# Optimization experiments

Hardware: AMD Instinct MI355X
Metric: run time of the kernel (lower is better)

The kernel has to match this reference:

```python
import jax, jax.numpy as jnp
import numpy as np

B = 1024      # batch
HG = 28       # grid side (28x28 image -> graph)
N = HG * HG   # 784 nodes per sample
K = 70        # node_sampled (relaxed categorical classes)
GCN_OUT = 48
H_DIM = 400
Z = 70
IMG = 784
TEMP = 0.5


def _grid_edges():
    idx = np.arange(N).reshape(HG, HG)
    src = np.concatenate([idx[:, :-1].ravel(), idx[:, 1:].ravel(), idx[:-1, :].ravel(), idx[1:, :].ravel()])
    dst = np.concatenate([idx[:, 1:].ravel(), idx[:, :-1].ravel(), idx[1:, :].ravel(), idx[:-1, :].ravel()])
    loop = np.arange(N)
    return (np.concatenate([src, loop]).astype(np.int32),
            np.concatenate([dst, loop]).astype(np.int32))


def _lin(key, fi, fo):
    kw, kb = jax.random.split(key)
    s = 1.0 / np.sqrt(fi)
    return (jax.random.uniform(kw, (fi, fo), jnp.float32, -s, s),
            jax.random.uniform(kb, (fo,), jnp.float32, -s, s))


def setup_inputs() -> dict:
    key = jax.random.key(0)
    ks = jax.random.split(key, 16)
    src, dst = _grid_edges()
    u = jax.random.uniform(ks[2], (B, N, K), jnp.float32, 1e-6, 1.0 - 1e-6)
    inp = {
        'nodes': jax.random.normal(ks[0], (B, N, 2), jnp.float32),
        'logits': jax.random.normal(ks[1], (B, N, K), jnp.float32),
        'gumbel': -jnp.log(-jnp.log(u)),
        'eps': jax.random.normal(ks[3], (B, Z), jnp.float32),
    }
    inp['W1'], inp['b1'] = _lin(ks[4], 2, 16)
    inp['W2'], inp['b2'] = _lin(ks[5], 16, 32)
    inp['W3'], inp['b3'] = _lin(ks[6], 32, GCN_OUT)
    inp['We1'], inp['be1'] = _lin(ks[7], K * GCN_OUT, H_DIM)
    inp['We2'], inp['be2'] = _lin(ks[8], H_DIM, H_DIM)
    inp['Wmu'], inp['bmu'] = _lin(ks[9], H_DIM, Z)
    inp['Wvar'], inp['bvar'] = _lin(ks[10], H_DIM, Z)
    inp['Wd1'], inp['bd1'] = _lin(ks[11], Z, H_DIM)
    inp['Wd2'], inp['bd2'] = _lin(ks[12], H_DIM, IMG)
    inp['edge_src'] = jnp.asarray(src)
    inp['edge_dst'] = jnp.asarray(dst)
    return inp


def reference(nodes, logits, gumbel, eps,
              W1, b1, W2, b2, W3, b3,
              We1, be1, We2, be2,
              Wmu, bmu, Wvar, bvar,
              Wd1, bd1, Wd2, bd2,
              edge_src, edge_dst):
    # symmetric GCN normalization with self loops (already in edge list)
    deg = jnp.zeros((N,), nodes.dtype).at[edge_dst].add(1.0)
    dinv = jax.lax.rsqrt(deg)
    norm = dinv[edge_src] * dinv[edge_dst]  # [E]

    def gcn(h, W, b):
        h = h @ W                                   # [B,N,Fout]
        msg = h[:, edge_src] * norm[None, :, None]  # gather + scale, [B,E,Fout]
        return jnp.zeros_like(h).at[:, edge_dst].add(msg) + b

    h = jax.nn.relu(gcn(nodes, W1, b1))
    h = jax.nn.relu(gcn(h, W2, b2))
    h = jax.nn.relu(gcn(h, W3, b3))            # [B,N,48]

    # RelaxedOneHotCategorical(temp=0.5).rsample() == gumbel-softmax
    sample = jax.nn.softmax((logits + gumbel) / TEMP, axis=-1)  # [B,N,K]
    g = jnp.einsum('bnk,bnf->bkf', sample, h).reshape(h.shape[0], K * GCN_OUT)

    # encoder MLP + reparameterize
    e = jax.nn.relu(g @ We1 + be1)
    e = jax.nn.relu(e @ We2 + be2)
    mu = e @ Wmu + bmu
    var = jax.nn.softplus(e @ Wvar + bvar)
    z = mu + eps * jnp.sqrt(var + 1e-10)

    # decoder
    d = jax.nn.relu(z @ Wd1 + bd1)
    x_rec = jax.nn.sigmoid(d @ Wd2 + bd2)      # [B,784]
    return x_rec
```

## Files before the change

### kernel.cpp

```cpp
#include <hip/hip_runtime.h>
#include <hip/hip_bf16.h>


#define BB 1024
#define HG 28
#define NN 784
#define KK 70
#define F3 48
#define HD 400
#define ZD 70
#define IMGD 784

typedef __hip_bfloat16 bf16;
typedef __attribute__((ext_vector_type(8))) short s8v;
typedef __attribute__((ext_vector_type(4))) float f32x4;

__device__ __forceinline__ float dinv_ij(int i, int j){
  int deg = 1 + (i>0) + (i<HG-1) + (j>0) + (j<HG-1);
  return rsqrtf((float)deg);
}

__device__ __forceinline__ unsigned pk2(float a, float b){
  union { bf16 h; unsigned short u; } ua, ub;
  ua.h = __float2bfloat16(a); ub.h = __float2bfloat16(b);
  return ((unsigned)ub.u << 16) | ua.u;
}

__device__ __forceinline__ short bfbits(float v){
  union { bf16 h; short s; } u; u.h = __float2bfloat16(v); return u.s;
}

#define SYNC_LDS() do {                                   \
    asm volatile("" ::: "memory");                        \
    asm volatile("s_waitcnt lgkmcnt(0)" ::: "memory");    \
    __builtin_amdgcn_s_barrier();                         \
    asm volatile("" ::: "memory");                        \
  } while(0)

__global__ __launch_bounds__(256, 2)
void gcn_fused(const float* __restrict__ nodes,
               const float* __restrict__ W1, const float* __restrict__ b1,
               const float* __restrict__ W2, const float* __restrict__ b2,
               const float* __restrict__ W3, const float* __restrict__ b3,
               bf16* __restrict__ h3){
  __shared__ __align__(16) char smem[73216];
  float* regA = (float*)smem;
  float* regB = (float*)(smem + 36288);
  float* wbuf = (float*)(smem + 64512);
  float* W1s = wbuf;          float* b1s = wbuf + 32;
  float* W2s = wbuf + 48;     float* b2s = wbuf + 560;
  float* W3s = wbuf + 592;    float* b3s = wbuf + 2128;

  int tid = threadIdx.x;
  if (tid < 32)  W1s[tid] = W1[tid];
  if (tid < 16)  b1s[tid] = b1[tid];
  for (int t = tid; t < 512;  t += 256) W2s[t] = W2[t];
  if (tid < 32)  b2s[tid] = b2[tid];
  for (int t = tid; t < 1536; t += 256) W3s[t] = W3[t];
  if (tid < 48)  b3s[tid] = b3[tid];

  int b = blockIdx.x >> 2, s = blockIdx.x & 3;
  int base3 = s*7;
  int base2 = base3 - 1;
  int base1 = base3 - 2;
  const float* nb = nodes + (size_t)b*NN*2;
  __syncthreads();

  {
    float* h1s = regA;
    for (int t = tid; t < 308; t += 256){
      int lr = t/28, j = t - lr*28;
      int r = base1 + lr;
      float o[16] __attribute__((aligned(16)));
      if (r < 0 || r >= HG){
        #pragma unroll
        for (int f=0; f<16; f++) o[f] = 0.f;
      } else {
        float dn = dinv_ij(r,j);
        float a0 = dn*nb[(r*HG+j)*2+0], a1 = dn*nb[(r*HG+j)*2+1];
        if (r > 0)   { float w=dinv_ij(r-1,j); a0 += w*nb[((r-1)*HG+j)*2]; a1 += w*nb[((r-1)*HG+j)*2+1]; }
        if (r < HG-1){ float w=dinv_ij(r+1,j); a0 += w*nb[((r+1)*HG+j)*2]; a1 += w*nb[((r+1)*HG+j)*2+1]; }
        if (j > 0)   { float w=dinv_ij(r,j-1); a0 += w*nb[(r*HG+j-1)*2];   a1 += w*nb[(r*HG+j-1)*2+1]; }
        if (j < HG-1){ float w=dinv_ij(r,j+1); a0 += w*nb[(r*HG+j+1)*2];   a1 += w*nb[(r*HG+j+1)*2+1]; }
        a0 *= dn; a1 *= dn;
        #pragma unroll
        for (int f=0; f<16; f++) o[f] = fmaxf(a0*W1s[f] + a1*W1s[16+f] + b1s[f], 0.f);
      }
      float* dst = h1s + t*20;
      #pragma unroll
      for (int qq=0; qq<4; qq++) *(float4*)(dst + 4*qq) = *(float4*)&o[4*qq];
    }
  }
  __syncthreads();

  if (tid < 252){
    const float* h1s = regA;
    float* agg1 = regB;
    int lr = tid/28, j = tid - lr*28;
    int r = base2 + lr;
    float o[16] __attribute__((aligned(16)));
    if (r < 0 || r >= HG){
      #pragma unroll
      for (int f=0; f<16; f++) o[f] = 0.f;
    } else {
      int ln = (lr+1)*28 + j;
      float dn = dinv_ij(r,j);
      float wu = dinv_ij(r-1,j), wd = dinv_ij(r+1,j);
      float wl = (j>0)    ? dinv_ij(r,j-1) : 0.f;
      float wr = (j<HG-1) ? dinv_ij(r,j+1) : 0.f;
      const float* pc = h1s + ln*20;
      #pragma unroll
      for (int qq=0; qq<4; qq++){
        float4 vc = *(const float4*)(pc + 4*qq);
        float4 vu = *(const float4*)(pc - 28*20 + 4*qq);
        float4 vd = *(const float4*)(pc + 28*20 + 4*qq);
        float4 vl = *(const float4*)(pc - 20 + 4*qq);
        float4 vr = *(const float4*)(pc + 20 + 4*qq);
        o[4*qq+0] = dn*(dn*vc.x + wu*vu.x + wd*vd.x + wl*vl.x + wr*vr.x);
        o[4*qq+1] = dn*(dn*vc.y + wu*vu.y + wd*vd.y + wl*vl.y + wr*vr.y);
        o[4*qq+2] = dn*(dn*vc.z + wu*vu.z + wd*vd.z + wl*vl.z + wr*vr.z);
        o[4*qq+3] = dn*(dn*vc.w + wu*vu.w + wd*vd.w + wl*vl.w + wr*vr.w);
      }
    }
    float* dst = agg1 + tid*20;
    #pragma unroll
    for (int qq=0; qq<4; qq++) *(float4*)(dst + 4*qq) = *(float4*)&o[4*qq];
  }
  __syncthreads();

  {
    const float* agg1 = regB;
    float* h2s = regA;
    int tx = tid & 7, ty = tid >> 3;
    float4 w2r[16];
    #pragma unroll
    for (int fi=0; fi<16; fi++) w2r[fi] = *(const float4*)&W2s[fi*32 + tx*4];
    float4 bb = *(const float4*)&b2s[tx*4];
    #pragma unroll
    for (int i=0; i<8; i++){
      int n = ty + 32*i;
      if (n < 252){
        float af[16] __attribute__((aligned(16)));
        const float* ap = agg1 + n*20;
        #pragma unroll
        for (int qq=0; qq<4; qq++) *(float4*)&af[4*qq] = *(const float4*)(ap + 4*qq);
        float4 acc = bb;
        #pragma unroll
        for (int fi=0; fi<16; fi++){
          float a = af[fi];
          acc.x += a*w2r[fi].x; acc.y += a*w2r[fi].y;
          acc.z += a*w2r[fi].z; acc.w += a*w2r[fi].w;
        }
        acc.x = fmaxf(acc.x,0.f); acc.y = fmaxf(acc.y,0.f);
        acc.z = fmaxf(acc.z,0.f); acc.w = fmaxf(acc.w,0.f);
        *(float4*)&h2s[n*36 + tx*4] = acc;
      }
    }
  }
  __syncthreads();

  if (tid < 196){
    const float* h2s = regA;
    float* agg2 = regB;
    int lr = tid/28, j = tid - lr*28;
    int r = base3 + lr;
    int ln = (lr+1)*28 + j;
    float dn = dinv_ij(r,j);
    float wu = dinv_ij(r-1,j), wd = dinv_ij(r+1,j);
    float wl = (j>0)    ? dinv_ij(r,j-1) : 0.f;
    float wr = (j<HG-1) ? dinv_ij(r,j+1) : 0.f;
    const float* pc = h2s + ln*36;
    float* dst = agg2 + tid*36;
    #pragma unroll
    for (int qq=0; qq<8; qq++){
      float4 vc = *(const float4*)(pc + 4*qq);
      float4 vu = *(const float4*)(pc - 28*36 + 4*qq);
      float4 vd = *(const float4*)(pc + 28*36 + 4*qq);
      float4 vl = *(const float4*)(pc - 36 + 4*qq);
      float4 vr = *(const float4*)(pc + 36 + 4*qq);
      float4 o;
      o.x = dn*(dn*vc.x + wu*vu.x + wd*vd.x + wl*vl.x + wr*vr.x);
      o.y = dn*(dn*vc.y + wu*vu.y + wd*vd.y + wl*vl.y + wr*vr.y);
      o.z = dn*(dn*vc.z + wu*vu.z + wd*vd.z + wl*vl.z + wr*vr.z);
      o.w = dn*(dn*vc.w + wu*vu.w + wd*vd.w + wl*vl.w + wr*vr.w);
      *(float4*)(dst + 4*qq) = o;
    }
  }
  __syncthreads();

  {
    bf16* h3buf = (bf16*)regA;
    if (tid < 252){
      const float* agg2 = regB;
      int tx = tid % 12, ty = tid / 12;
      float4 w3r[32];
      #pragma unroll
      for (int fi=0; fi<32; fi++) w3r[fi] = *(const float4*)&W3s[fi*48 + tx*4];
      float4 bb = *(const float4*)&b3s[tx*4];
      #pragma unroll
      for (int i=0; i<10; i++){
        int n = ty + 21*i;
        if (n < 196){
          float af[32] __attribute__((aligned(16)));
          const float* ap = agg2 + n*36;
          #pragma unroll
          for (int qq=0; qq<8; qq++) *(float4*)&af[4*qq] = *(const float4*)(ap + 4*qq);
          float4 acc = bb;
          #pragma unroll
          for (int fi=0; fi<32; fi++){
            float a = af[fi];
            acc.x += a*w3r[fi].x; acc.y += a*w3r[fi].y;
            acc.z += a*w3r[fi].z; acc.w += a*w3r[fi].w;
          }
          uint2 pv;
          pv.x = pk2(fmaxf(acc.x,0.f), fmaxf(acc.y,0.f));
          pv.y = pk2(fmaxf(acc.z,0.f), fmaxf(acc.w,0.f));
          *(uint2*)((char*)h3buf + n*112 + tx*8) = pv;
        }
      }
    }
  }
  __syncthreads();

  {
    const char* h3buf = (const char*)regA;
    uint4* dst = (uint4*)(h3 + ((size_t)b*NN + base3*28)*F3);
    for (int t = tid; t < 1176; t += 256){
      int n = t/6, gq = t - n*6;
      dst[t] = *(const uint4*)(h3buf + n*112 + gq*16);
    }
  }
}

__global__ __launch_bounds__(256, 4)
void einsum_mfma_kernel(const float* __restrict__ logits, const float* __restrict__ gumbel,
                        const bf16* __restrict__ h3, float* __restrict__ g){
  __shared__ __align__(16) unsigned smemS[7488];
  const int SLO = 2880, HTO = 5760;

  int b = blockIdx.x, tid = threadIdx.x;
  int l = tid & 63, w = tid >> 6;
  int n_loc = tid >> 2, q = tid & 3;
  int kstart = q << 4;
  int kcnt = (q < 3) ? 16 : 22;
  int kc2 = kcnt >> 1;
  int m_pair = tid >> 3;
  int half = (tid >> 2) & 1;
  int ks = w >> 1, mh = w & 1;
  int mtoff = mh ? 3 : 0, mtcnt = mh ? 2 : 3;

  for (int t = tid; t < 720; t += 256){
    int bb2 = t >= 360, r = t - bb2*360;
    if (bb2) smemS[SLO + 2520 + r] = 0u;
    else     smemS[2520 + r] = 0u;
  }

  f32x4 acc[3][3];
  #pragma unroll
  for (int mt=0; mt<3; mt++)
    #pragma unroll
    for (int bt=0; bt<3; bt++) acc[mt][bt] = (f32x4){0.f,0.f,0.f,0.f};

  float2 lx[11], gx[11];
  uint2 hA0, hB0, hA1, hB1;
  int hm0 = tid/12, hj0 = tid - hm0*12;
  int tt1 = tid + 256;
  int hm1 = tt1/12, hj1 = tt1 - hm1*12;

  auto issue_into = [&](int c){
    int c0 = c << 6;
    int node = c0 + n_loc;
    bool v = node < NN;
    const float* lp = logits + ((size_t)b*NN + node)*KK + kstart;
    const float* gp = gumbel + ((size_t)b*NN + node)*KK + kstart;
    int nld = (q < 3) ? 8 : 11;
    #pragma unroll
    for (int s=0; s<11; s++){
      bool a = v && (s < nld);
      lx[s] = a ? *(const float2*)(lp + 2*s) : (float2){0.f,0.f};
      gx[s] = a ? *(const float2*)(gp + 2*s) : (float2){0.f,0.f};
    }
    bool vA0 = (c0 + 2*hm0)     < NN;
    bool vB0 = (c0 + 2*hm0 + 1) < NN;
    const uint2* p0 = (const uint2*)(h3 + ((size_t)b*NN + c0 + 2*hm0)*F3 + 4*hj0);
    hA0 = vA0 ? p0[0]  : (uint2){0u,0u};
    hB0 = vB0 ? p0[12] : (uint2){0u,0u};
    if (tid < 128){
      bool vA1 = (c0 + 2*hm1)     < NN;
      bool vB1 = (c0 + 2*hm1 + 1) < NN;
      const uint2* p1 = (const uint2*)(h3 + ((size_t)b*NN + c0 + 2*hm1)*F3 + 4*hj1);
      hA1 = vA1 ? p1[0]  : (uint2){0u,0u};
      hB1 = vB1 ? p1[12] : (uint2){0u,0u};
    }
  };

  auto consume_pack = [&](int c){
    int c0 = c << 6;
    bool v = (c0 + n_loc) < NN;
    float x[22];
    #pragma unroll
    for (int s=0; s<11; s++){
      x[2*s]   = 2.f*(lx[s].x + gx[s].x);
      x[2*s+1] = 2.f*(lx[s].y + gx[s].y);
    }
    float mx = -1e30f;
    #pragma unroll
    for (int i=0; i<22; i++) if (i < kcnt) mx = fmaxf(mx, x[i]);
    mx = fmaxf(mx, __shfl_xor(mx, 1));
    mx = fmaxf(mx, __shfl_xor(mx, 2));
    float sum = 0.f;
    #pragma unroll
    for (int i=0; i<22; i++) if (i < kcnt){ x[i] = __expf(x[i]-mx); sum += x[i]; }
    sum += __shfl_xor(sum, 1);
    sum += __shfl_xor(sum, 2);
    float rs = v ? 1.0f/sum : 0.f;
    #pragma unroll
    for (int i=0; i<22; i++){
      if (i < kcnt){
        float p = x[i]*rs;
        unsigned hb = (unsigned)(unsigned short)bfbits(p);
        union { short s; bf16 h; } uh; uh.s = (short)hb;
        float lo = p - __bfloat162float(uh.h);
        unsigned lb = (unsigned)(unsigned short)bfbits(lo);
        unsigned phb = (unsigned)__shfl_xor((int)hb, 4);
        unsigned plb = (unsigned)__shfl_xor((int)lb, 4);
        unsigned dh = (half==0) ? (hb | (phb<<16)) : (phb | (hb<<16));
        unsigned dl = (half==0) ? (lb | (plb<<16)) : (plb | (lb<<16));
        bool doW = (half==0) ? (i < kc2) : (i >= kc2);
        if (doW){
          int k = kstart + i;
          int col = m_pair ^ (((k>>4)&3)<<3);
          smemS[k*36 + col] = dh;
          smemS[SLO + k*36 + col] = dl;
        }
      }
    }
    {
      unsigned d0 = (hA0.x & 0xFFFFu) | (hB0.x << 16);
      unsigned d1 = (hA0.x >> 16)     | (hB0.x & 0xFFFF0000u);
      unsigned d2 = (hA0.y & 0xFFFFu) | (hB0.y << 16);
      unsigned d3 = (hA0.y >> 16)     | (hB0.y & 0xFFFF0000u);
      #pragma unroll
      for (int i2=0; i2<4; i2++){
        int f = 4*hj0 + i2;
        int col = hm0 ^ (((f>>4)&3)<<3);
        unsigned dv = (i2==0)?d0:(i2==1)?d1:(i2==2)?d2:d3;
        smemS[HTO + f*36 + col] = dv;
      }
      if (tid < 128){
        unsigned e0 = (hA1.x & 0xFFFFu) | (hB1.x << 16);
        unsigned e1 = (hA1.x >> 16)     | (hB1.x & 0xFFFF0000u);
        unsigned e2 = (hA1.y & 0xFFFFu) | (hB1.y << 16);
        unsigned e3 = (hA1.y >> 16)     | (hB1.y & 0xFFFF0000u);
        #pragma unroll
        for (int i2=0; i2<4; i2++){
          int f = 4*hj1 + i2;
          int col = hm1 ^ (((f>>4)&3)<<3);
          unsigned dv = (i2==0)?e0:(i2==1)?e1:(i2==2)?e2:e3;
          smemS[HTO + f*36 + col] = dv;
        }
      }
    }
  };

  auto mfma_phase = [&](){
    int pr = (ks<<4) + ((l>>4)<<2);
    s8v Af[3], Al[3], Bf[3];
    #pragma unroll
    for (int mt=0; mt<3; mt++) if (mt < mtcnt){
      int row = (mtoff+mt)*16 + (l&15);
      int col = pr ^ (((row>>4)&3)<<3);
      Af[mt] = *(const s8v*)&smemS[row*36 + col];
      Al[mt] = *(const s8v*)&smemS[SLO + row*36 + col];
    }
    #pragma unroll
    for (int bt=0; bt<3; bt++){
      int f = bt*16 + (l&15);
      int col = pr ^ (((f>>4)&3)<<3);
      Bf[bt] = *(const s8v*)&smemS[HTO + f*36 + col];
    }
    #pragma unroll
    for (int mt=0; mt<3; mt++) if (mt < mtcnt)
      #pragma unroll
      for (int bt=0; bt<3; bt++){
        acc[mt][bt] = __builtin_amdgcn_mfma_f32_16x16x32_bf16(Af[mt], Bf[bt], acc[mt][bt], 0, 0, 0);
        acc[mt][bt] = __builtin_amdgcn_mfma_f32_16x16x32_bf16(Al[mt], Bf[bt], acc[mt][bt], 0, 0, 0);
      }
  };

  issue_into(0);
  consume_pack(0);
  issue_into(1);
  SYNC_LDS();

  for (int c = 0; c < 13; c++){
    mfma_phase();
    if (c < 12){
      SYNC_LDS();
      consume_pack(c+1);
      if (c + 2 <= 12) issue_into(c+2);
      SYNC_LDS();
    }
  }

  __syncthreads();
  float* cred = (float*)&smemS[0];
  if (ks == 0){
    #pragma unroll
    for (int mt=0; mt<3; mt++) if (mt < mtcnt)
      #pragma unroll
      for (int bt=0; bt<3; bt++)
        #pragma unroll
        for (int r=0; r<4; r++){
          int row = (mtoff+mt)*16 + (l>>4)*4 + r;
          int col = bt*16 + (l&15);
          cred[row*49 + col] = acc[mt][bt][r];
        }
  }
  __syncthreads();
  if (ks == 1){
    #pragma unroll
    for (int mt=0; mt<3; mt++) if (mt < mtcnt)
      #pragma unroll
      for (int bt=0; bt<3; bt++)
        #pragma unroll
        for (int r=0; r<4; r++){
          int row = (mtoff+mt)*16 + (l>>4)*4 + r;
          int col = bt*16 + (l&15);
          cred[row*49 + col] += acc[mt][bt][r];
        }
  }
  __syncthreads();
  for (int t = tid; t < KK*F3; t += 256){
    int r = t / F3, c2 = t - r*F3;
    g[(size_t)b*(KK*F3) + t] = cred[r*49 + c2];
  }
}

template<int ACT>
__global__ __launch_bounds__(256)
void dense_kernel(const float* __restrict__ A, const float* __restrict__ W,
                  const float* __restrict__ bias, float* __restrict__ out,
                  int M, int K, int Nn, int kChunk){
  __shared__ float As[16][65];
  __shared__ float Bs[16][64];
  int tx = threadIdx.x & 15, ty = threadIdx.x >> 4;
  int m0 = blockIdx.x*64, n0 = blockIdx.y*64;
  int ks = blockIdx.z * kChunk;
  int ke = min(K, ks + kChunk);
  int a_kk = threadIdx.x & 15, a_mm = threadIdx.x >> 4;
  int b_nn = threadIdx.x & 63, b_k0 = threadIdx.x >> 6;
  float ra[4], rb[4];
  float acc[4][4] = {};

  #pragma unroll
  for (int s=0; s<4; s++){
    int gk = ks + a_kk;
    ra[s] = (gk < ke) ? A[(size_t)(m0 + a_mm + s*16)*K + gk] : 0.f;
  }
  #pragma unroll
  for (int s=0; s<4; s++){
    int gk = ks + b_k0 + s*4, gn = n0 + b_nn;
    rb[s] = (gk < ke && gn < Nn) ? W[(size_t)gk*Nn + gn] : 0.f;
  }

  for (int k0 = ks; k0 < ke; k0 += 16){
    #pragma unroll
    for (int s=0; s<4; s++) As[a_kk][a_mm + s*16] = ra[s];
    #pragma unroll
    for (int s=0; s<4; s++) Bs[b_k0 + s*4][b_nn] = rb[s];
    __syncthreads();
    if (k0 + 16 < ke){
      #pragma unroll
      for (int s=0; s<4; s++){
        int gk = k0 + 16 + a_kk;
        ra[s] = (gk < ke) ? A[(size_t)(m0 + a_mm + s*16)*K + gk] : 0.f;
      }
      #pragma unroll
      for (int s=0; s<4; s++){
        int gk = k0 + 16 + b_k0 + s*4, gn = n0 + b_nn;
        rb[s] = (gk < ke && gn < Nn) ? W[(size_t)gk*Nn + gn] : 0.f;
      }
    }
    #pragma unroll
    for (int kk=0; kk<16; kk++){
      float a[4], bv[4];
      #pragma unroll
      for (int i2=0; i2<4; i2++) a[i2] = As[kk][ty*4+i2];
      #pragma unroll
      for (int j2=0; j2<4; j2++) bv[j2] = Bs[kk][tx*4+j2];
      #pragma unroll
      for (int i2=0; i2<4; i2++)
        #pragma unroll
        for (int j2=0; j2<4; j2++) acc[i2][j2] += a[i2]*bv[j2];
    }
    __syncthreads();
  }

  if (ACT == 2){
    float* po = out + (size_t)blockIdx.z*M*Nn;
    #pragma unroll
    for (int j2=0; j2<4; j2++){
      int gn = n0 + tx*4 + j2;
      if (gn < Nn){
        #pragma unroll
        for (int i2=0; i2<4; i2++)
          po[(size_t)(m0 + ty*4 + i2)*Nn + gn] = acc[i2][j2];
      }
    }
  } else {
    #pragma unroll
    for (int j2=0; j2<4; j2++){
      int gn = n0 + tx*4 + j2;
      if (gn < Nn){
        float bb = bias[gn];
        #pragma unroll
        for (int i2=0; i2<4; i2++){
          float v = acc[i2][j2] + bb;
          v = (ACT == 0) ? fmaxf(v, 0.f) : 1.0f/(1.0f + __expf(-v));
          out[(size_t)(m0 + ty*4 + i2)*Nn + gn] = v;
        }
      }
    }
  }
}

__global__ __launch_bounds__(256)
void dense_dualB_partial(const float* __restrict__ A, const float* __restrict__ Wmu,
                         const float* __restrict__ Wvar, float* __restrict__ out,
                         int M, int K, int Nn, int kChunk){
  __shared__ float As[16][65];
  __shared__ float Bs[16][64];
  int tx = threadIdx.x & 15, ty = threadIdx.x >> 4;
  int m0 = blockIdx.x*64, n0 = blockIdx.y*64;
  int ks = blockIdx.z * kChunk;
  int ke = min(K, ks + kChunk);
  int a_kk = threadIdx.x & 15, a_mm = threadIdx.x >> 4;
  int b_nn = threadIdx.x & 63, b_k0 = threadIdx.x >> 6;
  float ra[4], rb[4];
  float acc[4][4] = {};

  auto bload = [&](int gk, int gn)->float{
    if (gk >= ke || gn >= Nn) return 0.f;
    return (gn < ZD) ? Wmu[(size_t)gk*ZD + gn] : Wvar[(size_t)gk*ZD + gn - ZD];
  };

  #pragma unroll
  for (int s=0; s<4; s++){
    int gk = ks + a_kk;
    ra[s] = (gk < ke) ? A[(size_t)(m0 + a_mm + s*16)*K + gk] : 0.f;
  }
  #pragma unroll
  for (int s=0; s<4; s++) rb[s] = bload(ks + b_k0 + s*4, n0 + b_nn);

  for (int k0 = ks; k0 < ke; k0 += 16){
    #pragma unroll
    for (int s=0; s<4; s++) As[a_kk][a_mm + s*16] = ra[s];
    #pragma unroll
    for (int s=0; s<4; s++) Bs[b_k0 + s*4][b_nn] = rb[s];
    __syncthreads();
    if (k0 + 16 < ke){
      #pragma unroll
      for (int s=0; s<4; s++){
        int gk = k0 + 16 + a_kk;
        ra[s] = (gk < ke) ? A[(size_t)(m0 + a_mm + s*16)*K + gk] : 0.f;
      }
      #pragma unroll
      for (int s=0; s<4; s++) rb[s] = bload(k0 + 16 + b_k0 + s*4, n0 + b_nn);
    }
    #pragma unroll
    for (int kk=0; kk<16; kk++){
      float a[4], bv[4];
      #pragma unroll
      for (int i2=0; i2<4; i2++) a[i2] = As[kk][ty*4+i2];
      #pragma unroll
      for (int j2=0; j2<4; j2++) bv[j2] = Bs[kk][tx*4+j2];
      #pragma unroll
      for (int i2=0; i2<4; i2++)
        #pragma unroll
        for (int j2=0; j2<4; j2++) acc[i2][j2] += a[i2]*bv[j2];
    }
    __syncthreads();
  }

  float* po = out + (size_t)blockIdx.z*M*Nn;
  #pragma unroll
  for (int j2=0; j2<4; j2++){
    int gn = n0 + tx*4 + j2;
    if (gn < Nn){
      #pragma unroll
      for (int i2=0; i2<4; i2++)
        po[(size_t)(m0 + ty*4 + i2)*Nn + gn] = acc[i2][j2];
    }
  }
}

template<int ACT>
__global__ __launch_bounds__(256)
void reduce_bias_act(const float* __restrict__ part, const float* __restrict__ bias,
                     float* __restrict__ out, int M, int Nn, int S){
  int idx = blockIdx.x*256 + threadIdx.x;
  if (idx >= M*Nn) return;
  int n = idx % Nn;
  float s = bias[n];
  for (int i=0; i<S; i++) s += part[(size_t)i*M*Nn + idx];
  out[idx] = (ACT == 0) ? fmaxf(s, 0.f) : 1.0f/(1.0f + __expf(-s));
}

__global__ __launch_bounds__(256)
void reduce_reparam(const float* __restrict__ part, const float* __restrict__ bmu,
                    const float* __restrict__ bvar, const float* __restrict__ eps,
                    float* __restrict__ z, int S){
  int idx = blockIdx.x*256 + threadIdx.x;
  int b = idx / ZD, zi = idx - b*ZD;
  float mu = bmu[zi], va = bvar[zi];
  for (int s=0; s<S; s++){
    const float* pr = part + ((size_t)s*BB + b)*140;
    mu += pr[zi];
    va += pr[ZD + zi];
  }
  float sp = fmaxf(va, 0.f) + log1pf(__expf(-fabsf(va)));
  z[idx] = mu + eps[idx]*sqrtf(sp + 1e-10f);
}

extern "C" void kernel_launch(void* const* d_in, const int* in_sizes, int n_in,
                              void* d_out, int out_size, void* d_ws, size_t ws_size,
                              hipStream_t stream){
  (void)in_sizes; (void)n_in; (void)out_size; (void)ws_size;
  const float* nodes  = (const float*)d_in[0];
  const float* logits = (const float*)d_in[1];
  const float* gumbel = (const float*)d_in[2];
  const float* eps    = (const float*)d_in[3];
  const float* W1 =(const float*)d_in[4],  *b1 =(const float*)d_in[5];
  const float* W2 =(const float*)d_in[6],  *b2 =(const float*)d_in[7];
  const float* W3 =(const float*)d_in[8],  *b3 =(const float*)d_in[9];
  const float* We1=(const float*)d_in[10], *be1=(const float*)d_in[11];
  const float* We2=(const float*)d_in[12], *be2=(const float*)d_in[13];
  const float* Wmu=(const float*)d_in[14], *bmu=(const float*)d_in[15];
  const float* Wvr=(const float*)d_in[16], *bvr=(const float*)d_in[17];
  const float* Wd1=(const float*)d_in[18], *bd1=(const float*)d_in[19];
  const float* Wd2=(const float*)d_in[20], *bd2=(const float*)d_in[21];

  char* ws = (char*)d_ws;
  bf16*  h3 = (bf16*)(ws);
  float* g  = (float*)(ws + 77070336);
  float* e1 = (float*)(ws + 90832896);
  float* e2 = (float*)(ws + 92471296);
  float* zb = (float*)(ws + 94109696);
  float* dd = (float*)(ws + 94396416);
  float* part = (float*)(ws);
  float* out = (float*)d_out;

  gcn_fused<<<4096, 256, 0, stream>>>(nodes, W1, b1, W2, b2, W3, b3, h3);
  einsum_mfma_kernel<<<1024, 256, 0, stream>>>(logits, gumbel, h3, g);
  dense_kernel<2><<<dim3(16, 7, 8), 256, 0, stream>>>(g, We1, nullptr, part, 1024, 3360, 400, 432);
  reduce_bias_act<0><<<1600, 256, 0, stream>>>(part, be1, e1, 1024, 400, 8);
  dense_kernel<2><<<dim3(16, 7, 4), 256, 0, stream>>>(e1, We2, nullptr, part, 1024, 400, 400, 112);
  reduce_bias_act<0><<<1600, 256, 0, stream>>>(part, be2, e2, 1024, 400, 4);
  dense_dualB_partial<<<dim3(16, 3, 4), 256, 0, stream>>>(e2, Wmu, Wvr, part, 1024, 400, 140, 112);
  reduce_reparam<<<280, 256, 0, stream>>>(part, bmu, bvr, eps, zb, 4);
  dense_kernel<0><<<dim3(16, 7, 1), 256, 0, stream>>>(zb, Wd1, bd1, dd, 1024, 70, 400, 70);
  dense_kernel<2><<<dim3(16, 13, 4), 256, 0, stream>>>(dd, Wd2, nullptr, part, 1024, 400, 784, 112);
  reduce_bias_act<1><<<3136, 256, 0, stream>>>(part, bd2, out, 1024, 784, 4);
}
```

Before: 446.2 us.

## Remove register prefetch pipeline in einsum kernel and drop launch bounds

Removes the software prefetch that held the next chunk's logits, gumbel and h3 values in registers across the MFMA phase. Loads are now issued right before they are used inside consume_pack. The __launch_bounds__(256,4) hint is also dropped. This is meant to cut register pressure and raise occupancy, but the global load latency is no longer hidden behind the MFMA work.

```diff
diff --git a/kernel.cpp b/kernel.cpp
--- a/kernel.cpp
+++ b/kernel.cpp
@@ -232,7 +232,7 @@
   }
 }
 
-__global__ __launch_bounds__(256, 4)
+__global__
 void einsum_mfma_kernel(const float* __restrict__ logits, const float* __restrict__ gumbel,
                         const bf16* __restrict__ h3, float* __restrict__ g){
   __shared__ __align__(16) unsigned smemS[7488];
@@ -261,47 +261,25 @@
     #pragma unroll
     for (int bt=0; bt<3; bt++) acc[mt][bt] = (f32x4){0.f,0.f,0.f,0.f};
 
-  float2 lx[11], gx[11];
-  uint2 hA0, hB0, hA1, hB1;
   int hm0 = tid/12, hj0 = tid - hm0*12;
   int tt1 = tid + 256;
   int hm1 = tt1/12, hj1 = tt1 - hm1*12;
 
-  auto issue_into = [&](int c){
+  auto consume_pack = [&](int c){
     int c0 = c << 6;
     int node = c0 + n_loc;
     bool v = node < NN;
     const float* lp = logits + ((size_t)b*NN + node)*KK + kstart;
     const float* gp = gumbel + ((size_t)b*NN + node)*KK + kstart;
     int nld = (q < 3) ? 8 : 11;
+    float x[22];
     #pragma unroll
     for (int s=0; s<11; s++){
       bool a = v && (s < nld);
-      lx[s] = a ? *(const float2*)(lp + 2*s) : (float2){0.f,0.f};
-      gx[s] = a ? *(const float2*)(gp + 2*s) : (float2){0.f,0.f};
-    }
-    bool vA0 = (c0 + 2*hm0)     < NN;
-    bool vB0 = (c0 + 2*hm0 + 1) < NN;
-    const uint2* p0 = (const uint2*)(h3 + ((size_t)b*NN + c0 + 2*hm0)*F3 + 4*hj0);
-    hA0 = vA0 ? p0[0]  : (uint2){0u,0u};
-    hB0 = vB0 ? p0[12] : (uint2){0u,0u};
-    if (tid < 128){
-      bool vA1 = (c0 + 2*hm1)     < NN;
-      bool vB1 = (c0 + 2*hm1 + 1) < NN;
-      const uint2* p1 = (const uint2*)(h3 + ((size_t)b*NN + c0 + 2*hm1)*F3 + 4*hj1);
-      hA1 = vA1 ? p1[0]  : (uint2){0u,0u};
-      hB1 = vB1 ? p1[12] : (uint2){0u,0u};
-    }
-  };
-
-  auto consume_pack = [&](int c){
-    int c0 = c << 6;
-    bool v = (c0 + n_loc) < NN;
-    float x[22];
-    #pragma unroll
-    for (int s=0; s<11; s++){
-      x[2*s]   = 2.f*(lx[s].x + gx[s].x);
-      x[2*s+1] = 2.f*(lx[s].y + gx[s].y);
+      float2 lv = a ? *(const float2*)(lp + 2*s) : (float2){0.f,0.f};
+      float2 gv = a ? *(const float2*)(gp + 2*s) : (float2){0.f,0.f};
+      x[2*s]   = 2.f*(lv.x + gv.x);
+      x[2*s+1] = 2.f*(lv.y + gv.y);
     }
     float mx = -1e30f;
     #pragma unroll
@@ -336,6 +314,11 @@
       }
     }
     {
+      bool vA0 = (c0 + 2*hm0)     < NN;
+      bool vB0 = (c0 + 2*hm0 + 1) < NN;
+      const uint2* p0 = (const uint2*)(h3 + ((size_t)b*NN + c0 + 2*hm0)*F3 + 4*hj0);
+      uint2 hA0 = vA0 ? p0[0]  : (uint2){0u,0u};
+      uint2 hB0 = vB0 ? p0[12] : (uint2){0u,0u};
       unsigned d0 = (hA0.x & 0xFFFFu) | (hB0.x << 16);
       unsigned d1 = (hA0.x >> 16)     | (hB0.x & 0xFFFF0000u);
       unsigned d2 = (hA0.y & 0xFFFFu) | (hB0.y << 16);
@@ -348,6 +331,11 @@
         smemS[HTO + f*36 + col] = dv;
       }
       if (tid < 128){
+        bool vA1 = (c0 + 2*hm1)     < NN;
+        bool vB1 = (c0 + 2*hm1 + 1) < NN;
+        const uint2* p1 = (const uint2*)(h3 + ((size_t)b*NN + c0 + 2*hm1)*F3 + 4*hj1);
+        uint2 hA1 = vA1 ? p1[0]  : (uint2){0u,0u};
+        uint2 hB1 = vB1 ? p1[12] : (uint2){0u,0u};
         unsigned e0 = (hA1.x & 0xFFFFu) | (hB1.x << 16);
         unsigned e1 = (hA1.x >> 16)     | (hB1.x & 0xFFFF0000u);
         unsigned e2 = (hA1.y & 0xFFFFu) | (hB1.y << 16);
@@ -388,9 +376,7 @@
       }
   };
 
-  issue_into(0);
   consume_pack(0);
-  issue_into(1);
   SYNC_LDS();
 
   for (int c = 0; c < 13; c++){
@@ -398,7 +384,6 @@
     if (c < 12){
       SYNC_LDS();
       consume_pack(c+1);
-      if (c + 2 <= 12) issue_into(c+2);
       SYNC_LDS();
     }
   }
```

Result: faster. 400.9 us (median of 2 runs) (-10.1%).
